# Performance work log

Hardware: AMD Instinct MI355X
Metric: run time of the kernel (lower is better)

The kernel has to match this reference:

```python
import jax, jax.numpy as jnp
import numpy as np
import math

B, N0, DEG, D = 128, 1024, 16, 64
N = B * N0
E = N * DEG
K1 = math.ceil(0.8 * N0)   # 820
K2 = math.ceil(0.8 * K1)   # 656
K3 = math.ceil(0.8 * K2)   # 525


def _sage(x, src, dst, emask, W, b, U, n_nodes):
    # message = relu(lin(x_j)) is per-source-node, so compute once per node
    msg = jax.nn.relu(x @ W.T + b)                     # [n_nodes, D]
    m = jnp.where(emask[:, None], msg[src], -jnp.inf)  # [E, D]
    aggr = jax.ops.segment_max(m, dst, num_segments=n_nodes)
    aggr = jnp.maximum(aggr, msg)                      # add_self_loops under max-aggr
    return jax.nn.relu(jnp.concatenate([aggr, x], axis=1) @ U.T)


def _topk(x, src, dst, emask, p, n_per_graph, k):
    score = (x @ p) / jnp.linalg.norm(p)               # [B*n]
    topv, topi = jax.lax.top_k(score.reshape(B, n_per_graph), k)  # [B,k]
    perm = (topi + jnp.arange(B)[:, None] * n_per_graph).reshape(-1)
    new_x = x[perm] * jnp.tanh(topv).reshape(-1, 1)
    inv = jnp.full(B * n_per_graph, -1, dtype=src.dtype).at[perm].set(
        jnp.arange(B * k, dtype=src.dtype))
    ns, nd = inv[src], inv[dst]
    nmask = emask & (ns >= 0) & (nd >= 0)
    return new_x, jnp.maximum(ns, 0), jnp.maximum(nd, 0), nmask


def _readout(x, k):
    xb = x.reshape(B, k, D)
    return jnp.concatenate([xb.max(axis=1), xb.mean(axis=1)], axis=1)  # [B, 2D]


def _forward(x_ids, edge_index, emb, W1, b1, U1, p1, W2, b2, U2, p2,
             W3, b3, U3, p3, l1W, l1b, l2W, l2b, l3W, l3b):
    src, dst = edge_index[0], edge_index[1]
    emask = jnp.ones(E, dtype=bool)
    x = emb[x_ids]                                     # item_embedding + squeeze
    x = jax.nn.relu(_sage(x, src, dst, emask, W1, b1, U1, N))
    x, src, dst, emask = _topk(x, src, dst, emask, p1, N0, K1)
    x1 = _readout(x, K1)
    x = jax.nn.relu(_sage(x, src, dst, emask, W2, b2, U2, B * K1))
    x, src, dst, emask = _topk(x, src, dst, emask, p2, K1, K2)
    x2 = _readout(x, K2)
    x = jax.nn.relu(_sage(x, src, dst, emask, W3, b3, U3, B * K2))
    x, src, dst, emask = _topk(x, src, dst, emask, p3, K2, K3)
    x3 = _readout(x, K3)
    h = x1 + x2 + x3
    h = jax.nn.relu(h @ l1W.T + l1b)
    h = jax.nn.relu(h @ l2W.T + l2b)
    out = jax.nn.sigmoid(h @ l3W.T + l3b)              # [B, 64]; torch squeeze(1) is a no-op
    batch = jnp.repeat(jnp.arange(B, dtype=jnp.int32), K3)
    return out, batch


def setup_inputs():
    key = jax.random.key(0)
    ks = jax.random.split(key, 16)
    x_ids = jax.random.randint(ks[0], (N,), 0, 4, dtype=jnp.int32)
    off = jnp.repeat(jnp.arange(B, dtype=jnp.int32) * N0, E // B)
    src = jax.random.randint(ks[1], (E,), 0, N0, dtype=jnp.int32) + off
    dst = jax.random.randint(ks[2], (E,), 0, N0, dtype=jnp.int32) + off
    s = 0.1
    def lin(k, o, i):
        return jax.random.normal(k, (o, i), dtype=jnp.float32) * s
    return dict(
        x_ids=x_ids, edge_index=jnp.stack([src, dst]),
        emb=jax.random.normal(ks[3], (4, D), dtype=jnp.float32),
        W1=lin(ks[4], D, D), b1=jnp.zeros(D, jnp.float32), U1=lin(ks[5], D, 2 * D),
        p1=jax.random.normal(ks[6], (D,), dtype=jnp.float32),
        W2=lin(ks[7], D, D), b2=jnp.zeros(D, jnp.float32), U2=lin(ks[8], D, 2 * D),
        p2=jax.random.normal(ks[9], (D,), dtype=jnp.float32),
        W3=lin(ks[10], D, D), b3=jnp.zeros(D, jnp.float32), U3=lin(ks[11], D, 2 * D),
        p3=jax.random.normal(ks[12], (D,), dtype=jnp.float32),
        l1W=lin(ks[13], D, 2 * D), l1b=jnp.zeros(D, jnp.float32),
        l2W=lin(ks[14], D, D), l2b=jnp.zeros(D, jnp.float32),
        l3W=lin(ks[15], D, D), l3b=jnp.zeros(D, jnp.float32))


def reference(x_ids, edge_index, emb, W1, b1, U1, p1, W2, b2, U2, p2,
              W3, b3, U3, p3, l1W, l1b, l2W, l2b, l3W, l3b):
    return _forward(x_ids, edge_index, emb, W1, b1, U1, p1, W2, b2, U2, p2,
                    W3, b3, U3, p3, l1W, l1b, l2W, l2b, l3W, l3b)
```

## Files before the change

kernel.cpp:

```cpp
#include <hip/hip_runtime.h>
#include <hip/hip_bf16.h>
#include <math.h>

#define BGRAPH 128
#define NPER0 1024
#define DDIM 64
#define NTOT (BGRAPH*NPER0)
#define ETOT (NTOT*16)
#define EPG  (ETOT/BGRAPH)
#define KK1 820
#define KK2 656
#define KK3 525

__device__ __forceinline__ bool cmp_before(float va, int ia, float vb, int ib) {
    return (va > vb) || (va == vb && ia < ib);
}

__global__ void k_msg1_table(const float* __restrict__ emb, const float* __restrict__ W,
                             const float* __restrict__ b, float* __restrict__ msgT) {
    int id = blockIdx.x, d = threadIdx.x;
    float a = b[d];
    for (int k = 0; k < 64; k++) a = fmaf(emb[id * 64 + k], W[d * 64 + k], a);
    msgT[id * 64 + d] = fmaxf(a, 0.f);
}

__global__ void k_combo1_table(const float* __restrict__ msgT, const float* __restrict__ emb,
                               const float* __restrict__ U, const float* __restrict__ p,
                               float* __restrict__ s1T, float* __restrict__ x2T) {
    __shared__ float cat[128];
    int c = blockIdx.x, d = threadIdx.x;
    int mask = c >> 2, id = c & 3;
    float ag = -INFINITY;
    for (int i = 0; i < 4; i++) if (mask & (1 << i)) ag = fmaxf(ag, msgT[i * 64 + d]);
    if (mask == 0) ag = 0.f;
    cat[d] = ag; cat[64 + d] = emb[id * 64 + d];
    __syncthreads();
    float a = 0.f;
    for (int k = 0; k < 128; k++) a = fmaf(U[d * 128 + k], cat[k], a);
    a = fmaxf(a, 0.f);
    float pv = p[d];
    float nrm = pv * pv, sv = a * pv;
    #pragma unroll
    for (int o = 32; o > 0; o >>= 1) { nrm += __shfl_xor(nrm, o); sv += __shfl_xor(sv, o); }
    float sc = sv / sqrtf(nrm);
    if (d == 0) s1T[c] = sc;
    x2T[c * 64 + d] = a * tanhf(sc);
}

__global__ void k_msg2_table(const float* __restrict__ x2T, const float* __restrict__ W,
                             const float* __restrict__ b, float* __restrict__ msg2T) {
    int c = blockIdx.x, d = threadIdx.x;
    float a = b[d];
    for (int k = 0; k < 64; k++) a = fmaf(x2T[c * 64 + k], W[d * 64 + k], a);
    msg2T[c * 64 + d] = fmaxf(a, 0.f);
}

__global__ __launch_bounds__(1024) void k_mask_combo1(const int* __restrict__ eidx,
                                                      const int* __restrict__ ids,
                                                      const float* __restrict__ s1T,
                                                      int* __restrict__ combo1,
                                                      float* __restrict__ score) {
    __shared__ unsigned lmask[1024];
    __shared__ int lids[1024];
    int g = blockIdx.x, t = threadIdx.x;
    int nb = g * NPER0;
    lids[t] = ids[nb + t];
    lmask[t] = 0u;
    __syncthreads();
    const int* es = eidx + (size_t)g * EPG;
    const int* ed = eidx + ETOT + (size_t)g * EPG;
    for (int e = t; e < EPG; e += 1024)
        atomicOr(&lmask[ed[e] - nb], 1u << lids[es[e] - nb]);
    __syncthreads();
    int id = lids[t];
    int cb = (int)(((lmask[t] | (1u << id)) << 2) | (unsigned)id);
    combo1[nb + t] = cb;
    score[nb + t] = s1T[cb];
}

__global__ __launch_bounds__(1024) void k_topk(const float* __restrict__ score,
                                               int nper, int k,
                                               float* __restrict__ topv,
                                               int* __restrict__ topi,
                                               const int* __restrict__ rawsrc,
                                               const int* __restrict__ rawdst,
                                               const ushort2* __restrict__ ein2,
                                               const int* __restrict__ ecnt_in,
                                               ushort2* __restrict__ eout,
                                               int* __restrict__ ecnt_out,
                                               int mode) {
    __shared__ float sv[1024];
    __shared__ int   si[1024];
    __shared__ int   invl[1024];
    __shared__ int   scnt;
    int g = blockIdx.x, i = threadIdx.x;
    if (i == 0) scnt = 0;
    sv[i] = (i < nper) ? score[g * nper + i] : -INFINITY;
    si[i] = i;
    __syncthreads();
    float v = sv[i]; int ix = si[i];
    #pragma unroll
    for (int ksz = 2; ksz <= 64; ksz <<= 1) {
        bool up = (i & ksz) == 0;
        for (int j = ksz >> 1; j > 0; j >>= 1) {
            float ov = __shfl_xor(v, j);
            int   oi = __shfl_xor(ix, j);
            bool take = cmp_before(v, ix, ov, oi) ^ ((i & j) != 0) ^ (!up);
            if (!take) { v = ov; ix = oi; }
        }
    }
    sv[i] = v; si[i] = ix;
    __syncthreads();
    for (int ksz = 128; ksz <= 1024; ksz <<= 1) {
        bool up = (i & ksz) == 0;
        for (int j = ksz >> 1; j >= 64; j >>= 1) {
            int ixj = i ^ j;
            if (ixj > i) {
                float va = sv[i], vb = sv[ixj];
                int ia = si[i], ib = si[ixj];
                if (up != cmp_before(va, ia, vb, ib)) {
                    sv[i] = vb; sv[ixj] = va; si[i] = ib; si[ixj] = ia;
                }
            }
            __syncthreads();
        }
        v = sv[i]; ix = si[i];
        for (int j = 32; j > 0; j >>= 1) {
            float ov = __shfl_xor(v, j);
            int   oi = __shfl_xor(ix, j);
            bool take = cmp_before(v, ix, ov, oi) ^ ((i & j) != 0) ^ (!up);
            if (!take) { v = ov; ix = oi; }
        }
        sv[i] = v; si[i] = ix;
        __syncthreads();
    }
    if (i < k) { topv[g * 1024 + i] = sv[i]; topi[g * 1024 + i] = si[i]; }
    int s = si[i];
    if (s < nper) invl[s] = (i < k) ? i : -1;
    if (mode == 2) return;
    __syncthreads();
    int pcin = (mode == 0) ? EPG : ecnt_in[g];
    for (int e = i; e < pcin; e += 1024) {
        int ns, nd;
        if (mode == 0) {
            ns = invl[rawsrc[(size_t)g * EPG + e] - g * nper];
            nd = invl[rawdst[(size_t)g * EPG + e] - g * nper];
        } else {
            ushort2 sd = ein2[(size_t)g * EPG + e];
            if (sd.x == 0xFFFFu) continue;
            ns = invl[sd.x]; nd = invl[sd.y];
        }
        if (ns >= 0 && nd >= 0) {
            int pos = atomicAdd(&scnt, 1);
            eout[(size_t)g * EPG + pos] = make_ushort2((unsigned short)ns, (unsigned short)nd);
        }
    }
    __syncthreads();
    int cnt = scnt;
    int pc = (cnt + 1023) & ~1023;
    for (int e2 = cnt + i; e2 < pc; e2 += 1024)
        eout[(size_t)g * EPG + e2] = make_ushort2(0xFFFFu, 0);
    if (i == 0) ecnt_out[g] = pc;
}

__global__ __launch_bounds__(1024) void k_mask_aggr2(const ushort2* __restrict__ edges,
                                                     const int* __restrict__ ecnt,
                                                     const int* __restrict__ combo2,
                                                     const float4* __restrict__ msg2T4,
                                                     float4* __restrict__ aggr4) {
    __shared__ float4 tab[1024];
    __shared__ unsigned mlo[KK1], mhi[KK1];
    __shared__ int lcombo[KK1];
    int g = blockIdx.x, t = threadIdx.x;
    tab[t] = msg2T4[t];
    for (int i2 = t; i2 < KK1; i2 += 1024) {
        int c = combo2[g * KK1 + i2];
        lcombo[i2] = c;
        mlo[i2] = (c < 32) ? (1u << c) : 0u;
        mhi[i2] = (c < 32) ? 0u : (1u << (c - 32));
    }
    __syncthreads();
    const ushort2* eb = edges + (size_t)g * EPG;
    int pc = ecnt[g];
    for (int e = t; e < pc; e += 1024) {
        ushort2 sd = eb[e];
        if (sd.x != 0xFFFFu) {
            int c = lcombo[sd.x];
            if (c < 32) atomicOr(&mlo[sd.y], 1u << c);
            else        atomicOr(&mhi[sd.y], 1u << (c - 32));
        }
    }
    __syncthreads();
    for (int i2 = t; i2 < KK1 * 16; i2 += 1024) {
        int node = i2 >> 4, f = i2 & 15;
        unsigned lo = mlo[node], hi = mhi[node];
        float4 a = make_float4(-INFINITY, -INFINITY, -INFINITY, -INFINITY);
        while (lo) {
            int bb = __ffs(lo) - 1; lo &= lo - 1;
            float4 w = tab[bb * 16 + f];
            a.x = fmaxf(a.x, w.x); a.y = fmaxf(a.y, w.y);
            a.z = fmaxf(a.z, w.z); a.w = fmaxf(a.w, w.w);
        }
        while (hi) {
            int bb = __ffs(hi) - 1; hi &= hi - 1;
            float4 w = tab[(32 + bb) * 16 + f];
            a.x = fmaxf(a.x, w.x); a.y = fmaxf(a.y, w.y);
            a.z = fmaxf(a.z, w.z); a.w = fmaxf(a.w, w.w);
        }
        aggr4[((size_t)g * KK1 + node) * 16 + f] = a;
    }
}

__global__ __launch_bounds__(128) void k_dense64(const float* __restrict__ x,
                                                 const float* __restrict__ W,
                                                 const float* __restrict__ b,
                                                 float* __restrict__ out) {
    __shared__ float4 Wsh[64 * 16];
    int t = threadIdx.x;
    const float4* W4 = (const float4*)W;
    #pragma unroll
    for (int i = 0; i < 8; i++) Wsh[t + i * 128] = W4[t + i * 128];
    int node = blockIdx.x * 128 + t;
    float4 xr[16];
    const float4* xp = (const float4*)(x + (size_t)node * 64);
    #pragma unroll
    for (int i = 0; i < 16; i++) xr[i] = xp[i];
    __syncthreads();
    float4* op = (float4*)(out + (size_t)node * 64);
    #pragma unroll 1
    for (int d4 = 0; d4 < 16; d4++) {
        int d = d4 * 4;
        float a0 = b[d], a1 = b[d+1], a2 = b[d+2], a3 = b[d+3];
        #pragma unroll
        for (int kk = 0; kk < 16; kk++) {
            float4 xv = xr[kk];
            float4 w0 = Wsh[(d+0)*16+kk], w1 = Wsh[(d+1)*16+kk];
            float4 w2 = Wsh[(d+2)*16+kk], w3 = Wsh[(d+3)*16+kk];
            a0 = fmaf(w0.w,xv.w,fmaf(w0.z,xv.z,fmaf(w0.y,xv.y,fmaf(w0.x,xv.x,a0))));
            a1 = fmaf(w1.w,xv.w,fmaf(w1.z,xv.z,fmaf(w1.y,xv.y,fmaf(w1.x,xv.x,a1))));
            a2 = fmaf(w2.w,xv.w,fmaf(w2.z,xv.z,fmaf(w2.y,xv.y,fmaf(w2.x,xv.x,a2))));
            a3 = fmaf(w3.w,xv.w,fmaf(w3.z,xv.z,fmaf(w3.y,xv.y,fmaf(w3.x,xv.x,a3))));
        }
        op[d4] = make_float4(fmaxf(a0,0.f), fmaxf(a1,0.f), fmaxf(a2,0.f), fmaxf(a3,0.f));
    }
}

__global__ __launch_bounds__(128) void k_dense128cat(const float* __restrict__ aggr,
                                                     const float* __restrict__ x,
                                                     const float* __restrict__ U,
                                                     const float* __restrict__ p,
                                                     float* __restrict__ out,
                                                     float* __restrict__ score) {
    __shared__ float4 Ush[64 * 32];
    int t = threadIdx.x;
    const float4* U4 = (const float4*)U;
    #pragma unroll
    for (int i = 0; i < 16; i++) Ush[t + i * 128] = U4[t + i * 128];
    int node = blockIdx.x * 128 + t;
    float4 xr[32];
    const float4* ap = (const float4*)(aggr + (size_t)node * 64);
    const float4* xp = (const float4*)(x    + (size_t)node * 64);
    #pragma unroll
    for (int i = 0; i < 16; i++) xr[i] = ap[i];
    #pragma unroll
    for (int i = 0; i < 16; i++) xr[16 + i] = xp[i];
    float pv = p[t & 63];
    float nrm = pv * pv;
    #pragma unroll
    for (int o = 32; o > 0; o >>= 1) nrm += __shfl_xor(nrm, o);
    nrm = sqrtf(nrm);
    __syncthreads();
    float4* op = (float4*)(out + (size_t)node * 64);
    float sacc = 0.f;
    #pragma unroll 1
    for (int d4 = 0; d4 < 16; d4++) {
        int d = d4 * 4;
        float a0 = 0.f, a1 = 0.f, a2 = 0.f, a3 = 0.f;
        #pragma unroll
        for (int kk = 0; kk < 32; kk++) {
            float4 xv = xr[kk];
            float4 w0 = Ush[(d+0)*32+kk], w1 = Ush[(d+1)*32+kk];
            float4 w2 = Ush[(d+2)*32+kk], w3 = Ush[(d+3)*32+kk];
            a0 = fmaf(w0.w,xv.w,fmaf(w0.z,xv.z,fmaf(w0.y,xv.y,fmaf(w0.x,xv.x,a0))));
            a1 = fmaf(w1.w,xv.w,fmaf(w1.z,xv.z,fmaf(w1.y,xv.y,fmaf(w1.x,xv.x,a1))));
            a2 = fmaf(w2.w,xv.w,fmaf(w2.z,xv.z,fmaf(w2.y,xv.y,fmaf(w2.x,xv.x,a2))));
            a3 = fmaf(w3.w,xv.w,fmaf(w3.z,xv.z,fmaf(w3.y,xv.y,fmaf(w3.x,xv.x,a3))));
        }
        a0 = fmaxf(a0, 0.f); a1 = fmaxf(a1, 0.f);
        a2 = fmaxf(a2, 0.f); a3 = fmaxf(a3, 0.f);
        sacc = fmaf(a0, p[d], fmaf(a1, p[d+1], fmaf(a2, p[d+2], fmaf(a3, p[d+3], sacc))));
        op[d4] = make_float4(a0, a1, a2, a3);
    }
    score[node] = sacc / nrm;
}

__global__ __launch_bounds__(1024) void k_edge_max(const ushort2* __restrict__ edges,
                                                   const int* __restrict__ ecnt,
                                                   const float4* __restrict__ msg4,
                                                   float4* __restrict__ aggr4,
                                                   int nper) {
    extern __shared__ unsigned smax[];
    int g = blockIdx.x, q = blockIdx.y, t = threadIdx.x;
    int nodebase = g * nper;
    int q4 = q * 4;
    for (int i = t; i < nper * 4; i += 1024) {
        int node = i >> 2, dd = (i & 3) * 4;
        float4 vv = msg4[(size_t)(nodebase + node) * 16 + q4 + (i & 3)];
        int b0 = node << 4, sw = node & 15;
        smax[b0 | ((dd+0) ^ sw)] = __float_as_uint(vv.x);
        smax[b0 | ((dd+1) ^ sw)] = __float_as_uint(vv.y);
        smax[b0 | ((dd+2) ^ sw)] = __float_as_uint(vv.z);
        smax[b0 | ((dd+3) ^ sw)] = __float_as_uint(vv.w);
    }
    __syncthreads();
    const ushort2* eb = edges + (size_t)g * EPG;
    int pc = ecnt[g];
    int f4 = t & 3, d4 = f4 * 4, es = t >> 2;
    for (int base = 0; base < pc; base += 1024) {
        ushort2 sd[4];
        float4 vv[4];
        #pragma unroll
        for (int u = 0; u < 4; u++) sd[u] = eb[base + u * 256 + es];
        #pragma unroll
        for (int u = 0; u < 4; u++)
            vv[u] = (sd[u].x != 0xFFFFu)
                  ? msg4[(size_t)(nodebase + sd[u].x) * 16 + q4 + f4]
                  : make_float4(0.f, 0.f, 0.f, 0.f);
        #pragma unroll
        for (int u = 0; u < 4; u++) {
            if (sd[u].x != 0xFFFFu) {
                int ln = sd[u].y;
                int b0 = ln << 4, sw = ln & 15;
                atomicMax(&smax[b0 | ((d4+0) ^ sw)], __float_as_uint(vv[u].x));
                atomicMax(&smax[b0 | ((d4+1) ^ sw)], __float_as_uint(vv[u].y));
                atomicMax(&smax[b0 | ((d4+2) ^ sw)], __float_as_uint(vv[u].z));
                atomicMax(&smax[b0 | ((d4+3) ^ sw)], __float_as_uint(vv[u].w));
            }
        }
    }
    __syncthreads();
    for (int i = t; i < nper * 4; i += 1024) {
        int node = i >> 2, dd = (i & 3) * 4;
        int b0 = node << 4, sw = node & 15;
        float4 vv;
        vv.x = __uint_as_float(smax[b0 | ((dd+0) ^ sw)]);
        vv.y = __uint_as_float(smax[b0 | ((dd+1) ^ sw)]);
        vv.z = __uint_as_float(smax[b0 | ((dd+2) ^ sw)]);
        vv.w = __uint_as_float(smax[b0 | ((dd+3) ^ sw)]);
        aggr4[(size_t)(nodebase + node) * 16 + q4 + (i & 3)] = vv;
    }
}

__global__ __launch_bounds__(1024) void k_gather1(const int* __restrict__ combo1,
                                                  const float* __restrict__ x2T,
                                                  const int* __restrict__ topi,
                                                  float* __restrict__ xnew,
                                                  int* __restrict__ combo2,
                                                  float* __restrict__ r,
                                                  int nper, int k) {
    __shared__ float smx[16][64], ssm[16][64];
    int g = blockIdx.x, t = threadIdx.x;
    int d = t & 63, c16 = t >> 6;
    float m = -INFINITY, s = 0.f;
    for (int j = c16; j < k; j += 16) {
        int src = topi[g * 1024 + j];
        int cb = combo1[g * nper + src];
        float v = x2T[cb * 64 + d];
        xnew[((size_t)g * k + j) * 64 + d] = v;
        if (d == 0) combo2[g * k + j] = cb;
        m = fmaxf(m, v); s += v;
    }
    smx[c16][d] = m; ssm[c16][d] = s;
    __syncthreads();
    if (c16 == 0) {
        #pragma unroll
        for (int u = 1; u < 16; u++) { m = fmaxf(m, smx[u][d]); s += ssm[u][d]; }
        r[g * 128 + d] = m;
        r[g * 128 + 64 + d] = s / (float)k;
    }
}

__global__ __launch_bounds__(1024) void k_gather_readout(const float* __restrict__ x,
                                                         const float* __restrict__ topv,
                                                         const int* __restrict__ topi,
                                                         float* __restrict__ xnew,
                                                         float* __restrict__ r,
                                                         int nper, int k) {
    __shared__ float sscale[1024];
    __shared__ float smx[16][64], ssm[16][64];
    int g = blockIdx.x, t = threadIdx.x;
    if (t < k) sscale[t] = tanhf(topv[g * 1024 + t]);
    __syncthreads();
    int d = t & 63, c = t >> 6;
    float m = -INFINITY, s = 0.f;
    for (int j = c; j < k; j += 16) {
        int src = topi[g * 1024 + j];
        float v = x[((size_t)(g * nper) + src) * 64 + d] * sscale[j];
        xnew[((size_t)g * k + j) * 64 + d] = v;
        m = fmaxf(m, v); s += v;
    }
    smx[c][d] = m; ssm[c][d] = s;
    __syncthreads();
    if (c == 0) {
        #pragma unroll
        for (int u = 1; u < 16; u++) { m = fmaxf(m, smx[u][d]); s += ssm[u][d]; }
        r[g * 128 + d] = m;
        r[g * 128 + 64 + d] = s / (float)k;
    }
}

__global__ void k_mlp(const float* __restrict__ r1, const float* __restrict__ r2,
                      const float* __restrict__ r3,
                      const float* __restrict__ l1W, const float* __restrict__ l1b,
                      const float* __restrict__ l2W, const float* __restrict__ l2b,
                      const float* __restrict__ l3W, const float* __restrict__ l3b,
                      float* __restrict__ out) {
    __shared__ float h[128], h1[64], h2[64];
    int g = blockIdx.x, d = threadIdx.x;
    h[d]      = r1[g*128 + d]      + r2[g*128 + d]      + r3[g*128 + d];
    h[d + 64] = r1[g*128 + 64 + d] + r2[g*128 + 64 + d] + r3[g*128 + 64 + d];
    __syncthreads();
    float a = l1b[d];
    for (int k = 0; k < 128; k++) a = fmaf(l1W[d*128 + k], h[k], a);
    h1[d] = fmaxf(a, 0.f);
    __syncthreads();
    a = l2b[d];
    for (int k = 0; k < 64; k++) a = fmaf(l2W[d*64 + k], h1[k], a);
    h2[d] = fmaxf(a, 0.f);
    __syncthreads();
    a = l3b[d];
    for (int k = 0; k < 64; k++) a = fmaf(l3W[d*64 + k], h2[k], a);
    out[g*64 + d] = 1.f / (1.f + expf(-a));
}

__global__ void k_batch(float* __restrict__ out) {
    int i = blockIdx.x * blockDim.x + threadIdx.x;
    if (i < BGRAPH * KK3) out[i] = (float)(i / KK3);
}

extern "C" void kernel_launch(void* const* d_in, const int* in_sizes, int n_in,
                              void* d_out, int out_size, void* d_ws, size_t ws_size,
                              hipStream_t stream) {
    const int*   x_ids = (const int*)  d_in[0];
    const int*   eidx  = (const int*)  d_in[1];
    const float* emb   = (const float*)d_in[2];
    const float* W1 = (const float*)d_in[3];  const float* b1 = (const float*)d_in[4];
    const float* U1 = (const float*)d_in[5];  const float* p1 = (const float*)d_in[6];
    const float* W2 = (const float*)d_in[7];  const float* b2 = (const float*)d_in[8];
    const float* U2 = (const float*)d_in[9];  const float* p2 = (const float*)d_in[10];
    const float* W3 = (const float*)d_in[11]; const float* b3 = (const float*)d_in[12];
    const float* U3 = (const float*)d_in[13]; const float* p3 = (const float*)d_in[14];
    const float* l1W = (const float*)d_in[15]; const float* l1b = (const float*)d_in[16];
    const float* l2W = (const float*)d_in[17]; const float* l2b = (const float*)d_in[18];
    const float* l3W = (const float*)d_in[19]; const float* l3b = (const float*)d_in[20];

    float* ws    = (float*)d_ws;
    float* xA    = ws;
    float* xB    = xA + (size_t)NTOT * 64;
    float* xC    = xB + (size_t)NTOT * 64;
    float* score = xC + (size_t)NTOT * 64;
    float* topv  = score + NTOT;
    float* r1    = topv + BGRAPH * 1024;
    float* r2    = r1 + BGRAPH * 128;
    float* r3    = r2 + BGRAPH * 128;
    float* msgT  = r3 + BGRAPH * 128;
    float* s1T   = msgT + 256;
    float* x2T   = s1T + 64;
    float* msg2T = x2T + 4096;
    ushort2* edgesB = (ushort2*)(msg2T + 4096);
    ushort2* edgesA = edgesB + ETOT;
    int* topi   = (int*)(edgesA + ETOT);
    int* combo1 = topi + BGRAPH * 1024;
    int* combo2 = combo1 + NTOT;
    int* ecnt1  = combo2 + BGRAPH * KK1;
    int* ecnt2  = ecnt1 + BGRAPH;

    const int n2 = BGRAPH * KK1;
    const int n3 = BGRAPH * KK2;

    k_msg1_table<<<4, 64, 0, stream>>>(emb, W1, b1, msgT);
    k_combo1_table<<<64, 64, 0, stream>>>(msgT, emb, U1, p1, s1T, x2T);
    k_msg2_table<<<64, 64, 0, stream>>>(x2T, W2, b2, msg2T);
    k_mask_combo1<<<BGRAPH, 1024, 0, stream>>>(eidx, x_ids, s1T, combo1, score);
    k_topk<<<BGRAPH, 1024, 0, stream>>>(score, NPER0, KK1, topv, topi,
                                        eidx, eidx + ETOT, nullptr, nullptr,
                                        edgesB, ecnt1, 0);
    k_gather1<<<BGRAPH, 1024, 0, stream>>>(combo1, x2T, topi, xA, combo2, r1, NPER0, KK1);

    k_mask_aggr2<<<BGRAPH, 1024, 0, stream>>>(edgesB, ecnt1, combo2,
                                              (const float4*)msg2T, (float4*)xC);
    k_dense128cat<<<n2 / 128, 128, 0, stream>>>(xC, xA, U2, p2, xB, score);
    k_topk<<<BGRAPH, 1024, 0, stream>>>(score, KK1, KK2, topv, topi,
                                        nullptr, nullptr, edgesB, ecnt1,
                                        edgesA, ecnt2, 1);
    k_gather_readout<<<BGRAPH, 1024, 0, stream>>>(xB, topv, topi, xC, r2, KK1, KK2);

    k_dense64<<<n3 / 128, 128, 0, stream>>>(xC, W3, b3, xB);
    k_edge_max<<<dim3(BGRAPH, 4), 1024, KK2 * 16 * sizeof(float), stream>>>(
        edgesA, ecnt2, (const float4*)xB, (float4*)xA, KK2);
    k_dense128cat<<<n3 / 128, 128, 0, stream>>>(xA, xC, U3, p3, xB, score);
    k_topk<<<BGRAPH, 1024, 0, stream>>>(score, KK2, KK3, topv, topi,
                                        nullptr, nullptr, nullptr, nullptr,
                                        nullptr, nullptr, 2);
    k_gather_readout<<<BGRAPH, 1024, 0, stream>>>(xB, topv, topi, xA, r3, KK2, KK3);

    k_mlp<<<BGRAPH, 64, 0, stream>>>(r1, r2, r3, l1W, l1b, l2W, l2b, l3W, l3b, (float*)d_out);
    k_batch<<<(BGRAPH * KK3 + 255) / 256, 256, 0, stream>>>((float*)d_out + BGRAPH * DDIM);
}
```

Baseline: 401.8 us.

## Restructure dense layers to lane-per-output-feature with register-resident weights

The two dense kernels move from one thread per node with weights in shared memory to one wavefront per contiguous range of nodes. Each lane owns one output feature and keeps that weight row in registers. Each node's input row is loaded as a wave-uniform broadcast, and the score dot product becomes a cross-lane shuffle reduction. This removes LDS traffic and the large per-thread input register arrays, and it makes output stores coalesced. The cost is one serial pass over nodes per wave, plus a shuffle reduction and a single-lane score store for every node.

```diff
diff --git a/kernel.cpp b/kernel.cpp
--- a/kernel.cpp
+++ b/kernel.cpp
@@ -211,87 +211,82 @@
     }
 }
 
-__global__ __launch_bounds__(128) void k_dense64(const float* __restrict__ x,
+
+__global__ __launch_bounds__(256) void k_dense64(const float* __restrict__ x,
                                                  const float* __restrict__ W,
                                                  const float* __restrict__ b,
-                                                 float* __restrict__ out) {
-    __shared__ float4 Wsh[64 * 16];
-    int t = threadIdx.x;
-    const float4* W4 = (const float4*)W;
+                                                 float* __restrict__ out, int n) {
+    int lane = threadIdx.x & 63;
+    int wid  = __builtin_amdgcn_readfirstlane(blockIdx.x * 4 + (threadIdx.x >> 6));
+    float4 w[16];
+    const float4* W4 = (const float4*)(W + lane * 64);
     #pragma unroll
-    for (int i = 0; i < 8; i++) Wsh[t + i * 128] = W4[t + i * 128];
-    int node = blockIdx.x * 128 + t;
-    float4 xr[16];
-    const float4* xp = (const float4*)(x + (size_t)node * 64);
-    #pragma unroll
-    for (int i = 0; i < 16; i++) xr[i] = xp[i];
-    __syncthreads();
-    float4* op = (float4*)(out + (size_t)node * 64);
-    #pragma unroll 1
-    for (int d4 = 0; d4 < 16; d4++) {
-        int d = d4 * 4;
-        float a0 = b[d], a1 = b[d+1], a2 = b[d+2], a3 = b[d+3];
+    for (int i = 0; i < 16; i++) w[i] = W4[i];
+    float bl = b[lane];
+    int nwaves = gridDim.x * 4;
+    int chunk = (n + nwaves - 1) / nwaves;
+    int n0 = wid * chunk;
+    int n1 = n0 + chunk; if (n1 > n) n1 = n;
+    for (int node = n0; node < n1; node++) {
+        const float4* x4 = (const float4*)(x + (size_t)node * 64);
+        float a0 = 0.f, a1 = 0.f, a2 = 0.f, a3 = 0.f;
         #pragma unroll
         for (int kk = 0; kk < 16; kk++) {
-            float4 xv = xr[kk];
-            float4 w0 = Wsh[(d+0)*16+kk], w1 = Wsh[(d+1)*16+kk];
-            float4 w2 = Wsh[(d+2)*16+kk], w3 = Wsh[(d+3)*16+kk];
-            a0 = fmaf(w0.w,xv.w,fmaf(w0.z,xv.z,fmaf(w0.y,xv.y,fmaf(w0.x,xv.x,a0))));
-            a1 = fmaf(w1.w,xv.w,fmaf(w1.z,xv.z,fmaf(w1.y,xv.y,fmaf(w1.x,xv.x,a1))));
-            a2 = fmaf(w2.w,xv.w,fmaf(w2.z,xv.z,fmaf(w2.y,xv.y,fmaf(w2.x,xv.x,a2))));
-            a3 = fmaf(w3.w,xv.w,fmaf(w3.z,xv.z,fmaf(w3.y,xv.y,fmaf(w3.x,xv.x,a3))));
-        }
-        op[d4] = make_float4(fmaxf(a0,0.f), fmaxf(a1,0.f), fmaxf(a2,0.f), fmaxf(a3,0.f));
-    }
-}
-
-__global__ __launch_bounds__(128) void k_dense128cat(const float* __restrict__ aggr,
+            float4 xv = x4[kk];
+            float4 wv = w[kk];
+            a0 = fmaf(wv.x, xv.x, a0); a1 = fmaf(wv.y, xv.y, a1);
+            a2 = fmaf(wv.z, xv.z, a2); a3 = fmaf(wv.w, xv.w, a3);
+        }
+        out[(size_t)node * 64 + lane] = fmaxf(((a0 + a1) + (a2 + a3)) + bl, 0.f);
+    }
+}
+
+__global__ __launch_bounds__(256) void k_dense128cat(const float* __restrict__ aggr,
                                                      const float* __restrict__ x,
                                                      const float* __restrict__ U,
                                                      const float* __restrict__ p,
                                                      float* __restrict__ out,
-                                                     float* __restrict__ score) {
-    __shared__ float4 Ush[64 * 32];
-    int t = threadIdx.x;
-    const float4* U4 = (const float4*)U;
+                                                     float* __restrict__ score, int n) {
+    int lane = threadIdx.x & 63;
+    int wid  = __builtin_amdgcn_readfirstlane(blockIdx.x * 4 + (threadIdx.x >> 6));
+    float4 w[32];
+    const float4* U4 = (const float4*)(U + lane * 128);
     #pragma unroll
-    for (int i = 0; i < 16; i++) Ush[t + i * 128] = U4[t + i * 128];
-    int node = blockIdx.x * 128 + t;
-    float4 xr[32];
-    const float4* ap = (const float4*)(aggr + (size_t)node * 64);
-    const float4* xp = (const float4*)(x    + (size_t)node * 64);
-    #pragma unroll
-    for (int i = 0; i < 16; i++) xr[i] = ap[i];
-    #pragma unroll
-    for (int i = 0; i < 16; i++) xr[16 + i] = xp[i];
-    float pv = p[t & 63];
+    for (int i = 0; i < 32; i++) w[i] = U4[i];
+    float pv = p[lane];
     float nrm = pv * pv;
     #pragma unroll
     for (int o = 32; o > 0; o >>= 1) nrm += __shfl_xor(nrm, o);
     nrm = sqrtf(nrm);
-    __syncthreads();
-    float4* op = (float4*)(out + (size_t)node * 64);
-    float sacc = 0.f;
-    #pragma unroll 1
-    for (int d4 = 0; d4 < 16; d4++) {
-        int d = d4 * 4;
+    int nwaves = gridDim.x * 4;
+    int chunk = (n + nwaves - 1) / nwaves;
+    int n0 = wid * chunk;
+    int n1 = n0 + chunk; if (n1 > n) n1 = n;
+    for (int node = n0; node < n1; node++) {
+        const float4* a4 = (const float4*)(aggr + (size_t)node * 64);
+        const float4* x4 = (const float4*)(x + (size_t)node * 64);
         float a0 = 0.f, a1 = 0.f, a2 = 0.f, a3 = 0.f;
         #pragma unroll
-        for (int kk = 0; kk < 32; kk++) {
-            float4 xv = xr[kk];
-            float4 w0 = Ush[(d+0)*32+kk], w1 = Ush[(d+1)*32+kk];
-            float4 w2 = Ush[(d+2)*32+kk], w3 = Ush[(d+3)*32+kk];
-            a0 = fmaf(w0.w,xv.w,fmaf(w0.z,xv.z,fmaf(w0.y,xv.y,fmaf(w0.x,xv.x,a0))));
-            a1 = fmaf(w1.w,xv.w,fmaf(w1.z,xv.z,fmaf(w1.y,xv.y,fmaf(w1.x,xv.x,a1))));
-            a2 = fmaf(w2.w,xv.w,fmaf(w2.z,xv.z,fmaf(w2.y,xv.y,fmaf(w2.x,xv.x,a2))));
-            a3 = fmaf(w3.w,xv.w,fmaf(w3.z,xv.z,fmaf(w3.y,xv.y,fmaf(w3.x,xv.x,a3))));
-        }
-        a0 = fmaxf(a0, 0.f); a1 = fmaxf(a1, 0.f);
-        a2 = fmaxf(a2, 0.f); a3 = fmaxf(a3, 0.f);
-        sacc = fmaf(a0, p[d], fmaf(a1, p[d+1], fmaf(a2, p[d+2], fmaf(a3, p[d+3], sacc))));
-        op[d4] = make_float4(a0, a1, a2, a3);
-    }
-    score[node] = sacc / nrm;
+        for (int kk = 0; kk < 16; kk++) {
+            float4 xv = a4[kk];
+            float4 wv = w[kk];
+            a0 = fmaf(wv.x, xv.x, a0); a1 = fmaf(wv.y, xv.y, a1);
+            a2 = fmaf(wv.z, xv.z, a2); a3 = fmaf(wv.w, xv.w, a3);
+        }
+        #pragma unroll
+        for (int kk = 0; kk < 16; kk++) {
+            float4 xv = x4[kk];
+            float4 wv = w[16 + kk];
+            a0 = fmaf(wv.x, xv.x, a0); a1 = fmaf(wv.y, xv.y, a1);
+            a2 = fmaf(wv.z, xv.z, a2); a3 = fmaf(wv.w, xv.w, a3);
+        }
+        float h = fmaxf((a0 + a1) + (a2 + a3), 0.f);
+        float sa = h * pv;
+        #pragma unroll
+        for (int o = 32; o > 0; o >>= 1) sa += __shfl_xor(sa, o);
+        out[(size_t)node * 64 + lane] = h;
+        if (lane == 0) score[node] = sa / nrm;
+    }
 }
 
 __global__ __launch_bounds__(1024) void k_edge_max(const ushort2* __restrict__ edges,
@@ -489,16 +484,16 @@
 
     k_mask_aggr2<<<BGRAPH, 1024, 0, stream>>>(edgesB, ecnt1, combo2,
                                               (const float4*)msg2T, (float4*)xC);
-    k_dense128cat<<<n2 / 128, 128, 0, stream>>>(xC, xA, U2, p2, xB, score);
+    k_dense128cat<<<512, 256, 0, stream>>>(xC, xA, U2, p2, xB, score, n2);
     k_topk<<<BGRAPH, 1024, 0, stream>>>(score, KK1, KK2, topv, topi,
                                         nullptr, nullptr, edgesB, ecnt1,
                                         edgesA, ecnt2, 1);
     k_gather_readout<<<BGRAPH, 1024, 0, stream>>>(xB, topv, topi, xC, r2, KK1, KK2);
 
-    k_dense64<<<n3 / 128, 128, 0, stream>>>(xC, W3, b3, xB);
+    k_dense64<<<512, 256, 0, stream>>>(xC, W3, b3, xB, n3);
     k_edge_max<<<dim3(BGRAPH, 4), 1024, KK2 * 16 * sizeof(float), stream>>>(
         edgesA, ecnt2, (const float4*)xB, (float4*)xA, KK2);
-    k_dense128cat<<<n3 / 128, 128, 0, stream>>>(xA, xC, U3, p3, xB, score);
+    k_dense128cat<<<512, 256, 0, stream>>>(xA, xC, U3, p3, xB, score, n3);
     k_topk<<<BGRAPH, 1024, 0, stream>>>(score, KK2, KK3, topv, topi,
                                         nullptr, nullptr, nullptr, nullptr,
                                         nullptr, nullptr, 2);
```

Result: slower. 515.6 us (+28.3%).
